# Performance work log

Hardware: AMD Instinct MI355X
Metric: run time of the kernel (lower is better)

The kernel has to match this reference:

```python
import jax, jax.numpy as jnp
import numpy as np

B, S, D, C_IN = 8, 1024, 512, 7
INNER = 2 * D              # mLSTM up-projection (proj_factor=2)
NH_M, DH_M = 4, INNER // 4 # mLSTM heads = n_heads//2
NH_S, DH_S = 8, D // 8     # sLSTM heads = n_heads
K_M, K_S = 7, 4            # conv kernels: enc_in, factor
FF = int(1.1 * D)          # sLSTM gated-FFN dim (proj_factor=1.1)
EPS = 1e-6
NEG = -1e30


def _ln(x, w):
    mu = x.mean(-1, keepdims=True)
    var = x.var(-1, keepdims=True)
    return (x - mu) * jax.lax.rsqrt(var + 1e-5) * w


def _headnorm(h, w):
    # h: [B,S,NH,DH] -> per-head groupnorm -> [B,S,NH*DH] * w
    mu = h.mean(-1, keepdims=True)
    var = h.var(-1, keepdims=True)
    hn = (h - mu) * jax.lax.rsqrt(var + 1e-5)
    b, s = h.shape[:2]
    return hn.reshape(b, s, -1) * w


def _causal_conv1d(x, w, b):
    # depthwise causal conv. x: [B,S,C], w: [C,k], b: [C]
    k = w.shape[1]
    xp = jnp.pad(x, ((0, 0), (k - 1, 0), (0, 0))).transpose(0, 2, 1)  # [B,C,S+k-1]
    y = jax.lax.conv_general_dilated(
        xp, w[:, None, :], (1,), 'VALID',
        dimension_numbers=('NCH', 'OIH', 'NCH'),
        feature_group_count=w.shape[0])
    return y.transpose(0, 2, 1) + b


def _mlstm_parallel(q, k, v, i_pre, f_pre):
    # q,k,v: [B,NH,S,DH]; i_pre,f_pre: [B,NH,S]. Stabilized parallel mLSTM cell.
    s = q.shape[2]
    logf = jax.nn.log_sigmoid(f_pre)
    cum = jnp.concatenate([jnp.zeros_like(logf[:, :, :1]), jnp.cumsum(logf, -1)], -1)  # [B,NH,S+1]
    dmat = cum[:, :, 1:, None] - cum[:, :, None, 1:]            # [B,NH,S,S]
    mask = jnp.tril(jnp.ones((s, s), bool))
    dmat = jnp.where(mask, dmat, NEG) + i_pre[:, :, None, :]    # add igate along keys
    m = dmat.max(-1, keepdims=True)                              # stabilizer
    Dm = jnp.exp(dmat - m)
    qk = jnp.einsum('bhqd,bhkd->bhqk', q, k) * (q.shape[-1] ** -0.5)
    C = qk * Dm
    n = jnp.maximum(jnp.abs(C.sum(-1, keepdims=True)), jnp.exp(-m)) + EPS
    return jnp.einsum('bhqk,bhkd->bhqd', C / n, v)               # [B,NH,S,DH]


def _forward(x_enc, x_mark_enc, x_dec, x_mark_dec, W_in, b_in,
             m_ln_w, m_Wup, m_bup, m_conv_w, m_conv_b, m_Wq, m_Wk, m_Wv,
             m_Wi, m_bi, m_Wf, m_bf, m_norm_w, m_skip, m_Wdown, m_bdown,
             s_ln_w, s_conv_w, s_conv_b, s_Wi, s_Wf, s_Wz, s_Wo,
             s_Ri, s_Rf, s_Rz, s_Ro, s_bi, s_bf, s_bz, s_bo, s_norm_w,
             s_ffn_ln_w, s_Wff_up, s_bff_up, s_Wff_down, s_bff_down,
             post_norm_w, W_out, b_out):
    b, s, _ = x_enc.shape
    x = x_enc @ W_in + b_in                                    # [B,S,D]

    # ---- block 0: mLSTM block ----
    res = x
    xn = _ln(x, m_ln_w)
    xm, z = jnp.split(xn @ m_Wup + m_bup, 2, axis=-1)          # each [B,S,INNER]
    conv = jax.nn.silu(_causal_conv1d(xm, m_conv_w, m_conv_b))
    qf, kf, vf = conv @ m_Wq, conv @ m_Wk, xm @ m_Wv
    gate_in = jnp.concatenate([qf, kf, vf], -1)                # [B,S,3*INNER]
    i_pre = (gate_in @ m_Wi + m_bi).transpose(0, 2, 1)         # [B,NH,S]
    f_pre = (gate_in @ m_Wf + m_bf).transpose(0, 2, 1)
    to_h = lambda t: t.reshape(b, s, NH_M, DH_M).transpose(0, 2, 1, 3)
    h = _mlstm_parallel(to_h(qf), to_h(kf), to_h(vf), i_pre, f_pre)
    h = h.transpose(0, 2, 1, 3)                                # [B,S,NH,DH]
    h = _headnorm(h, m_norm_w) + m_skip * conv                 # learnable skip
    x = res + (h * jax.nn.silu(z)) @ m_Wdown + m_bdown

    # ---- block 1: sLSTM block + gated FFN ----
    res = x
    xn = _ln(x, s_ln_w)
    conv = jax.nn.silu(_causal_conv1d(xn, s_conv_w, s_conv_b))
    gh = lambda t: t.reshape(b, s, NH_S, DH_S).transpose(1, 0, 2, 3)  # time-major
    gi, gf = gh(conv @ s_Wi + s_bi), gh(conv @ s_Wf + s_bf)
    gz, go = gh(xn @ s_Wz + s_bz), gh(xn @ s_Wo + s_bo)

    def step(carry, xs):
        c, n, m, hp = carry
        xi, xf, xz, xo = xs
        rec = lambda R: jnp.einsum('bhd,hde->bhe', hp, R)      # block-diag recurrent
        it, ft = xi + rec(s_Ri), xf + rec(s_Rf)
        zt, ot = xz + rec(s_Rz), xo + rec(s_Ro)
        m_new = jnp.maximum(ft + m, it)                        # exp-gate stabilizer
        ig = jnp.exp(it - m_new)
        fg = jnp.exp(ft + m - m_new)
        c_new = fg * c + ig * jnp.tanh(zt)
        n_new = fg * n + ig
        h_new = jax.nn.sigmoid(ot) * c_new / jnp.maximum(n_new, EPS)
        return (c_new, n_new, m_new, h_new), h_new

    z0 = jnp.zeros((b, NH_S, DH_S), x.dtype)
    _, hs = jax.lax.scan(step, (z0, z0, z0, z0), (gi, gf, gz, go))
    x = res + _headnorm(hs.transpose(1, 0, 2, 3), s_norm_w)

    res = x
    a, g = jnp.split(_ln(x, s_ffn_ln_w) @ s_Wff_up + s_bff_up, 2, axis=-1)
    x = res + (jax.nn.gelu(a) * g) @ s_Wff_down + s_bff_down

    x = _ln(x, post_norm_w)                                    # post-blocks norm
    return x @ W_out + b_out                                   # [B,S,7]


def setup_inputs() -> dict:
    key = jax.random.key(0)
    ks = iter(jax.random.split(key, 64))
    rn = lambda shape, sc=0.02: jax.random.normal(next(ks), shape, jnp.float32) * sc
    return {
        'x_enc': jax.random.normal(next(ks), (B, S, C_IN), jnp.float32),
        'x_mark_enc': jax.random.normal(next(ks), (B, S, 4), jnp.float32),
        'x_dec': jax.random.normal(next(ks), (B, S, C_IN), jnp.float32),
        'x_mark_dec': jax.random.normal(next(ks), (B, S, 4), jnp.float32),
        'W_in': rn((C_IN, D)), 'b_in': jnp.zeros((D,)),
        'm_ln_w': jnp.ones((D,)),
        'm_Wup': rn((D, 2 * INNER)), 'm_bup': jnp.zeros((2 * INNER,)),
        'm_conv_w': rn((INNER, K_M), 0.1), 'm_conv_b': jnp.zeros((INNER,)),
        'm_Wq': rn((INNER, INNER)), 'm_Wk': rn((INNER, INNER)), 'm_Wv': rn((INNER, INNER)),
        'm_Wi': rn((3 * INNER, NH_M)), 'm_bi': jnp.zeros((NH_M,)),
        'm_Wf': rn((3 * INNER, NH_M)), 'm_bf': jnp.full((NH_M,), 3.0),
        'm_norm_w': jnp.ones((INNER,)), 'm_skip': jnp.ones((INNER,)),
        'm_Wdown': rn((INNER, D)), 'm_bdown': jnp.zeros((D,)),
        's_ln_w': jnp.ones((D,)),
        's_conv_w': rn((D, K_S), 0.1), 's_conv_b': jnp.zeros((D,)),
        's_Wi': rn((D, D)), 's_Wf': rn((D, D)), 's_Wz': rn((D, D)), 's_Wo': rn((D, D)),
        's_Ri': rn((NH_S, DH_S, DH_S)), 's_Rf': rn((NH_S, DH_S, DH_S)),
        's_Rz': rn((NH_S, DH_S, DH_S)), 's_Ro': rn((NH_S, DH_S, DH_S)),
        's_bi': jnp.zeros((D,)), 's_bf': jnp.linspace(3.0, 6.0, D),
        's_bz': jnp.zeros((D,)), 's_bo': jnp.zeros((D,)),
        's_norm_w': jnp.ones((D,)),
        's_ffn_ln_w': jnp.ones((D,)),
        's_Wff_up': rn((D, 2 * FF)), 's_bff_up': jnp.zeros((2 * FF,)),
        's_Wff_down': rn((FF, D)), 's_bff_down': jnp.zeros((D,)),
        'post_norm_w': jnp.ones((D,)),
        'W_out': rn((D, C_IN)), 'b_out': jnp.zeros((C_IN,)),
    }


def reference(x_enc, x_mark_enc, x_dec, x_mark_dec, W_in, b_in,
              m_ln_w, m_Wup, m_bup, m_conv_w, m_conv_b, m_Wq, m_Wk, m_Wv,
              m_Wi, m_bi, m_Wf, m_bf, m_norm_w, m_skip, m_Wdown, m_bdown,
              s_ln_w, s_conv_w, s_conv_b, s_Wi, s_Wf, s_Wz, s_Wo,
              s_Ri, s_Rf, s_Rz, s_Ro, s_bi, s_bf, s_bz, s_bo, s_norm_w,
              s_ffn_ln_w, s_Wff_up, s_bff_up, s_Wff_down, s_bff_down,
              post_norm_w, W_out, b_out):
    return _forward(x_enc, x_mark_enc, x_dec, x_mark_dec, W_in, b_in,
                    m_ln_w, m_Wup, m_bup, m_conv_w, m_conv_b, m_Wq, m_Wk, m_Wv,
                    m_Wi, m_bi, m_Wf, m_bf, m_norm_w, m_skip, m_Wdown, m_bdown,
                    s_ln_w, s_conv_w, s_conv_b, s_Wi, s_Wf, s_Wz, s_Wo,
                    s_Ri, s_Rf, s_Rz, s_Ro, s_bi, s_bf, s_bz, s_bo, s_norm_w,
                    s_ffn_ln_w, s_Wff_up, s_bff_up, s_Wff_down, s_bff_down,
                    post_norm_w, W_out, b_out)
```

## Files before the change

### kernel.cpp

```cpp
#include <hip/hip_runtime.h>
#include <hip/hip_bf16.h>
#include <math.h>

typedef __hip_bfloat16 bf16;
typedef __attribute__((ext_vector_type(4))) float f32x4;
typedef __attribute__((ext_vector_type(8))) short bf16x8;
typedef __attribute__((ext_vector_type(8))) unsigned short u16x8;

#define DEV static __device__ __forceinline__

DEV float b2f(bf16 x) { return __bfloat162float(x); }
DEV bf16 f2b(float x) { return __float2bfloat16(x); }
DEV unsigned short f2us(float x) { bf16 h = __float2bfloat16(x); return *reinterpret_cast<unsigned short*>(&h); }
DEV float us2f(unsigned short u) { unsigned v = (unsigned)u << 16; float f; __builtin_memcpy(&f, &v, 4); return f; }

DEV float loadw(const void* p, size_t i, int bf) {
  return bf ? __bfloat162float(((const bf16*)p)[i]) : ((const float*)p)[i];
}

DEV float wredsum(float v) {
#pragma unroll
  for (int off = 32; off > 0; off >>= 1) v += __shfl_xor(v, off);
  return v;
}

DEV void gload_lds16(const void* g, void* l) {
  __builtin_amdgcn_global_load_lds((const __attribute__((address_space(1))) char*)g,
                                   (__attribute__((address_space(3))) char*)l, 16, 0, 0);
}

__global__ void k_flag(const unsigned* __restrict__ w1, int* flag) {
  if (threadIdx.x == 0 && blockIdx.x == 0) *flag = (*w1 == 0x3F800000u) ? 0 : 1;
}

__global__ void k_transpose(const void* __restrict__ W, int ldw, int colOff, bf16* __restrict__ Wt,
                            int K, int N, int Kpad, int Npad, const int* __restrict__ fp) {
  int bf = *fp;
  __shared__ float t[32][33];
  int n0 = blockIdx.x * 32, k0 = blockIdx.y * 32;
  int tx = threadIdx.x & 31, ty = threadIdx.x >> 5;
  for (int i = ty; i < 32; i += 8) {
    int k = k0 + i, n = n0 + tx;
    t[i][tx] = (k < K && n < N) ? loadw(W, (size_t)k * ldw + colOff + n, bf) : 0.f;
  }
  __syncthreads();
  for (int i = ty; i < 32; i += 8) {
    int n = n0 + i, k = k0 + tx;
    if (n < Npad && k < Kpad) Wt[(size_t)n * Kpad + k] = f2b(t[tx][i]);
  }
}

template <int RES>
__global__ __launch_bounds__(256) void k_gemm(
    const bf16* __restrict__ A, int lda, const bf16* __restrict__ Bt, int ldb,
    bf16* __restrict__ Cout, int ldc, const bf16* __restrict__ Res,
    const void* __restrict__ bias, int biasOff, int Nreal, int K,
    const int* __restrict__ fp) {
  int bf = *fp;
  __shared__ bf16 As[128 * 32];
  __shared__ bf16 Bs[128 * 32];
  int tid = threadIdx.x, wv = tid >> 6, lane = tid & 63;
  int mBase = blockIdx.y * 128, nBase = blockIdx.x * 128;
  int wm = (wv & 1) * 64, wn = (wv >> 1) * 64;
  f32x4 acc[4][4];
#pragma unroll
  for (int i = 0; i < 4; i++)
#pragma unroll
    for (int j = 0; j < 4; j++) acc[i][j] = 0.f;
  int r0 = (wv * 2) * 16 + (lane >> 2);
  int r1 = (wv * 2 + 1) * 16 + (lane >> 2);
  int cc = (lane & 3) * 8;
  const bf16* a0 = A + (size_t)(mBase + r0) * lda + cc;
  const bf16* a1 = A + (size_t)(mBase + r1) * lda + cc;
  const bf16* b0 = Bt + (size_t)(nBase + r0) * ldb + cc;
  const bf16* b1 = Bt + (size_t)(nBase + r1) * ldb + cc;
  for (int kt = 0; kt < K; kt += 32) {
    __syncthreads();
    gload_lds16(a0 + kt, As + (wv * 2) * 512);
    gload_lds16(a1 + kt, As + (wv * 2 + 1) * 512);
    gload_lds16(b0 + kt, Bs + (wv * 2) * 512);
    gload_lds16(b1 + kt, Bs + (wv * 2 + 1) * 512);
    __syncthreads();
    bf16x8 af[4], bfr[4];
#pragma unroll
    for (int i = 0; i < 4; i++) {
      af[i] = *(const bf16x8*)(As + (wm + i * 16 + (lane & 15)) * 32 + (lane >> 4) * 8);
      bfr[i] = *(const bf16x8*)(Bs + (wn + i * 16 + (lane & 15)) * 32 + (lane >> 4) * 8);
    }
#pragma unroll
    for (int i = 0; i < 4; i++)
#pragma unroll
      for (int j = 0; j < 4; j++)
        acc[i][j] = __builtin_amdgcn_mfma_f32_16x16x32_bf16(af[i], bfr[j], acc[i][j], 0, 0, 0);
  }
#pragma unroll
  for (int i = 0; i < 4; i++) {
#pragma unroll
    for (int j = 0; j < 4; j++) {
      int n = nBase + wn + j * 16 + (lane & 15);
      if (n < Nreal) {
        float bv = bias ? loadw(bias, biasOff + n, bf) : 0.f;
#pragma unroll
        for (int r = 0; r < 4; r++) {
          int m = mBase + wm + i * 16 + (lane >> 4) * 4 + r;
          float v = acc[i][j][r] + bv;
          if (RES) v += b2f(Res[(size_t)m * 512 + n]);
          Cout[(size_t)m * ldc + n] = f2b(v);
        }
      }
    }
  }
}

__global__ __launch_bounds__(256) void k_embed_ln(
    const void* __restrict__ xe, const void* __restrict__ Wi, const void* __restrict__ bi,
    const void* __restrict__ lw, bf16* __restrict__ x, bf16* __restrict__ xn,
    const int* __restrict__ fp) {
  int bf = *fp;
  int lane = threadIdx.x & 63, wv = threadIdx.x >> 6;
  size_t row = blockIdx.x * 4 + wv;
  float e[7];
#pragma unroll
  for (int c = 0; c < 7; c++) e[c] = loadw(xe, row * 7 + c, bf);
  float v[8];
#pragma unroll
  for (int j = 0; j < 8; j++) {
    int d = j * 64 + lane;
    float a = loadw(bi, d, bf);
#pragma unroll
    for (int c = 0; c < 7; c++) a += e[c] * loadw(Wi, c * 512 + d, bf);
    v[j] = a;
  }
  float s = 0, s2 = 0;
#pragma unroll
  for (int j = 0; j < 8; j++) { s += v[j]; s2 += v[j] * v[j]; }
  s = wredsum(s); s2 = wredsum(s2);
  float mu = s * (1.f / 512.f);
  float var = s2 * (1.f / 512.f) - mu * mu;
  float rq = rsqrtf(fmaxf(var, 0.f) + 1e-5f);
#pragma unroll
  for (int j = 0; j < 8; j++) {
    int d = j * 64 + lane;
    x[row * 512 + d] = f2b(v[j]);
    xn[row * 512 + d] = f2b((v[j] - mu) * rq * loadw(lw, d, bf));
  }
}

template <int KW>
__global__ void k_conv(const bf16* __restrict__ X, int ldx, int c4shift,
                       const void* __restrict__ cw, const void* __restrict__ cb,
                       bf16* __restrict__ out, int C, const int* __restrict__ fp) {
  int bf = *fp;
  int idx = blockIdx.x * 256 + threadIdx.x;
  int r = idx >> c4shift;
  int c4 = (idx & ((1 << c4shift) - 1)) * 4;
  int b = r >> 10, s = r & 1023;
  float a[4];
#pragma unroll
  for (int t = 0; t < 4; t++) a[t] = loadw(cb, c4 + t, bf);
#pragma unroll
  for (int j = 0; j < KW; j++) {
    int sj = s - (KW - 1) + j;
    if (sj >= 0) {
      const bf16* px = X + ((size_t)(b << 10) + sj) * ldx + c4;
#pragma unroll
      for (int t = 0; t < 4; t++) a[t] += b2f(px[t]) * loadw(cw, (c4 + t) * KW + j, bf);
    }
  }
#pragma unroll
  for (int t = 0; t < 4; t++) {
    float v = a[t];
    v = v / (1.f + __expf(-v));
    out[(size_t)r * C + c4 + t] = f2b(v);
  }
}

__global__ __launch_bounds__(256) void k_mgates(
    const bf16* __restrict__ qf, const bf16* __restrict__ kf, const bf16* __restrict__ vf,
    const void* __restrict__ Wi, const void* __restrict__ bi,
    const void* __restrict__ Wf, const void* __restrict__ bfv,
    float* __restrict__ ipre, float* __restrict__ fpre, const int* __restrict__ fp) {
  int bf = *fp;
  int lane = threadIdx.x & 63, wv = threadIdx.x >> 6;
  int row = blockIdx.x * 4 + wv;
  int b = row >> 10, s = row & 1023;
  float ai[4] = {0, 0, 0, 0}, af[4] = {0, 0, 0, 0};
  const bf16* srcs[3] = {qf + (size_t)row * 1024, kf + (size_t)row * 1024, vf + (size_t)row * 1024};
#pragma unroll
  for (int p = 0; p < 3; p++) {
    const bf16* sp = srcs[p];
#pragma unroll
    for (int it = 0; it < 16; it++) {
      int d = it * 64 + lane;
      float g = b2f(sp[d]);
      size_t wr = (size_t)(p * 1024 + d) * 4;
#pragma unroll
      for (int h = 0; h < 4; h++) {
        ai[h] += g * loadw(Wi, wr + h, bf);
        af[h] += g * loadw(Wf, wr + h, bf);
      }
    }
  }
#pragma unroll
  for (int h = 0; h < 4; h++) { ai[h] = wredsum(ai[h]); af[h] = wredsum(af[h]); }
  if (lane == 0) {
#pragma unroll
    for (int h = 0; h < 4; h++) {
      ipre[(size_t)(b * 4 + h) * 1024 + s] = ai[h] + loadw(bi, h, bf);
      fpre[(size_t)(b * 4 + h) * 1024 + s] = af[h] + loadw(bfv, h, bf);
    }
  }
}

__global__ void k_mprep(const float* __restrict__ ipre, const float* __restrict__ fpre,
                        float* __restrict__ aq, float* __restrict__ bk, float* __restrict__ bmax) {
  int bh = blockIdx.x, lane = threadIdx.x;
  float cum = 0.f, rmax = -3.4e38f;
  for (int t = 0; t < 1024; t += 64) {
    float f = fpre[(size_t)bh * 1024 + t + lane];
    float lf = fminf(f, 0.f) - log1pf(__expf(-fabsf(f)));
    float sc = lf;
#pragma unroll
    for (int off = 1; off < 64; off <<= 1) {
      float o = __shfl_up(sc, off);
      if (lane >= off) sc += o;
    }
    float a = cum + sc;
    float bkv = ipre[(size_t)bh * 1024 + t + lane] - a;
    float mx = bkv;
#pragma unroll
    for (int off = 1; off < 64; off <<= 1) {
      float o = __shfl_up(mx, off);
      if (lane >= off) mx = fmaxf(mx, o);
    }
    float m = fmaxf(rmax, mx);
    aq[(size_t)bh * 1024 + t + lane] = a;
    bk[(size_t)bh * 1024 + t + lane] = bkv;
    bmax[(size_t)bh * 1024 + t + lane] = m;
    cum += __shfl(sc, 63);
    rmax = fmaxf(rmax, __shfl(mx, 63));
  }
}

__global__ void k_vtrans(const bf16* __restrict__ vf, bf16* __restrict__ vt) {
  __shared__ bf16 t[32][33];
  int s0 = blockIdx.x * 32, d0 = blockIdx.y * 32, bh = blockIdx.z;
  int b = bh >> 2, h = bh & 3;
  int tx = threadIdx.x & 31, ty = threadIdx.x >> 5;
  for (int i = ty; i < 32; i += 8)
    t[i][tx] = vf[((size_t)(b << 10) + s0 + i) * 1024 + h * 256 + d0 + tx];
  __syncthreads();
  for (int i = ty; i < 32; i += 8)
    vt[((size_t)bh * 256 + d0 + i) * 1024 + s0 + tx] = t[tx][i];
}

__global__ __launch_bounds__(256) void k_mlstm(
    const bf16* __restrict__ qf, const bf16* __restrict__ kf, const bf16* __restrict__ vt,
    const float* __restrict__ aq, const float* __restrict__ bk, const float* __restrict__ bmax,
    const bf16* __restrict__ conv, const void* __restrict__ nw, const void* __restrict__ skip,
    bf16* __restrict__ y, const int* __restrict__ fp) {
  int bf = *fp;
  __shared__ bf16 Ks[64 * 256];
  __shared__ bf16 Vs[256 * 64];
  __shared__ unsigned short Ps[4][1024];
  int qt = blockIdx.x, bh = blockIdx.y;
  int b = bh >> 2, h = bh & 3;
  int tid = threadIdx.x, wv = tid >> 6, lane = tid & 63;
  size_t rowbase = (size_t)b << 10;
  int qw = qt * 64 + wv * 16;
  bf16x8 qreg[8];
  {
    const bf16* qp = qf + (rowbase + qw + (lane & 15)) * 1024 + h * 256 + (lane >> 4) * 8;
#pragma unroll
    for (int ck = 0; ck < 8; ck++) qreg[ck] = *(const bf16x8*)(qp + ck * 32);
  }
  float bmq[4], aqv[4];
#pragma unroll
  for (int r = 0; r < 4; r++) {
    int qg = qw + (lane >> 4) * 4 + r;
    bmq[r] = bmax[(size_t)bh * 1024 + qg];
    aqv[r] = aq[(size_t)bh * 1024 + qg];
  }
  f32x4 oacc[16];
#pragma unroll
  for (int i = 0; i < 16; i++) oacc[i] = 0.f;
  float rs[4] = {0, 0, 0, 0};
  int nkt = qt + 1;
  for (int kt = 0; kt < nkt; kt++) {
    int kbase = kt * 64;
    __syncthreads();
#pragma unroll
    for (int j = 0; j < 8; j++) {
      int ch = wv * 8 + j;
      int krow = ch * 2 + (lane >> 5);
      int sunit = (lane & 31) ^ (krow & 7);
      gload_lds16(kf + (rowbase + kbase + krow) * 1024 + h * 256 + sunit * 8, Ks + ch * 512);
    }
#pragma unroll
    for (int j = 0; j < 8; j++) {
      int ch = wv * 8 + j;
      int drow = ch * 8 + (lane >> 3);
      int sunit = (lane & 7) ^ (drow & 7);
      gload_lds16(vt + ((size_t)bh * 256 + drow) * 1024 + kbase + sunit * 8, Vs + ch * 512);
    }
    __syncthreads();
    float bkl = bk[(size_t)bh * 1024 + kbase + lane];
    f32x4 sacc[4];
#pragma unroll
    for (int kfg = 0; kfg < 4; kfg++) {
      int krow = kfg * 16 + (lane & 15);
      const char* kp = (const char*)Ks + krow * 512;
      int swz = (krow & 7) << 4;
      f32x4 sa = 0.f;
#pragma unroll
      for (int ck = 0; ck < 8; ck++) {
        int cb = (ck * 32 + (lane >> 4) * 8) * 2;
        bf16x8 bb = *(const bf16x8*)(kp + (cb ^ swz));
        sa = __builtin_amdgcn_mfma_f32_16x16x32_bf16(qreg[ck], bb, sa, 0, 0, 0);
      }
      sacc[kfg] = sa;
    }
    int qr0 = (lane >> 4) * 4;
#pragma unroll
    for (int kfg = 0; kfg < 4; kfg++) {
      int kloc = kfg * 16 + (lane & 15);
      float bkv = __shfl(bkl, kloc);
      int kglob = kbase + kloc;
#pragma unroll
      for (int r = 0; r < 4; r++) {
        int qloc = qr0 + r;
        int qglob = qt * 64 + wv * 16 + qloc;
        float p = sacc[kfg][r] * 0.0625f * __expf(bkv - bmq[r]);
        if (kglob > qglob) p = 0.f;
        rs[r] += p;
        int boff = qloc * 128 + ((kloc * 2) ^ ((qloc & 7) << 4));
        Ps[wv][boff >> 1] = f2us(p);
      }
    }
    __syncthreads();
#pragma unroll
    for (int kc = 0; kc < 2; kc++) {
      int qloc = lane & 15;
      int pboff = qloc * 128 + (((kc * 32 + (lane >> 4) * 8) * 2) ^ ((qloc & 7) << 4));
      bf16x8 pa = *(const bf16x8*)((const char*)Ps[wv] + pboff);
#pragma unroll
      for (int nf = 0; nf < 16; nf++) {
        int dr = nf * 16 + (lane & 15);
        int vboff = dr * 128 + (((kc * 32 + (lane >> 4) * 8) * 2) ^ ((dr & 7) << 4));
        bf16x8 vb = *(const bf16x8*)((const char*)Vs + vboff);
        oacc[nf] = __builtin_amdgcn_mfma_f32_16x16x32_bf16(pa, vb, oacc[nf], 0, 0, 0);
      }
    }
  }
#pragma unroll
  for (int r = 0; r < 4; r++) {
#pragma unroll
    for (int off = 1; off < 16; off <<= 1) rs[r] += __shfl_xor(rs[r], off);
  }
  float invn[4], mu[4], rqv[4];
#pragma unroll
  for (int r = 0; r < 4; r++) {
    float m = aqv[r] + bmq[r];
    float n = fmaxf(fabsf(rs[r]), __expf(-m)) + 1e-6f;
    invn[r] = 1.f / n;
  }
#pragma unroll
  for (int r = 0; r < 4; r++) {
    float s = 0.f, s2 = 0.f;
#pragma unroll
    for (int nf = 0; nf < 16; nf++) {
      float x = oacc[nf][r] * invn[r];
      s += x; s2 += x * x;
    }
#pragma unroll
    for (int off = 1; off < 16; off <<= 1) { s += __shfl_xor(s, off); s2 += __shfl_xor(s2, off); }
    mu[r] = s * (1.f / 256.f);
    float var = s2 * (1.f / 256.f) - mu[r] * mu[r];
    rqv[r] = rsqrtf(fmaxf(var, 0.f) + 1e-5f);
  }
#pragma unroll
  for (int nf = 0; nf < 16; nf++) {
    int dcol = h * 256 + nf * 16 + (lane & 15);
    float nwv = loadw(nw, dcol, bf);
    float skv = loadw(skip, dcol, bf);
#pragma unroll
    for (int r = 0; r < 4; r++) {
      size_t row = rowbase + qw + (lane >> 4) * 4 + r;
      float hn = (oacc[nf][r] * invn[r] - mu[r]) * rqv[r];
      float cv = b2f(conv[row * 1024 + dcol]);
      y[row * 1024 + dcol] = f2b(hn * nwv + skv * cv);
    }
  }
}

__global__ void k_zgate(bf16* __restrict__ y, const bf16* __restrict__ z) {
  size_t idx = ((size_t)blockIdx.x * 256 + threadIdx.x) * 8;
  u16x8 yv = *(const u16x8*)(y + idx);
  u16x8 zv = *(const u16x8*)(z + idx);
#pragma unroll
  for (int e = 0; e < 8; e++) {
    float f = us2f(yv[e]);
    float zz = us2f(zv[e]);
    f *= zz / (1.f + __expf(-zz));
    yv[e] = f2us(f);
  }
  *(u16x8*)(y + idx) = yv;
}

__global__ __launch_bounds__(256) void k_ln512(const bf16* __restrict__ X,
                                               const void* __restrict__ w,
                                               bf16* __restrict__ out,
                                               const int* __restrict__ fp) {
  int bf = *fp;
  int lane = threadIdx.x & 63, wv = threadIdx.x >> 6;
  size_t row = blockIdx.x * 4 + wv;
  float v[8];
  u16x8 q = *(const u16x8*)(X + row * 512 + lane * 8);
#pragma unroll
  for (int t = 0; t < 8; t++) v[t] = us2f(q[t]);
  float s = 0, s2 = 0;
#pragma unroll
  for (int t = 0; t < 8; t++) { s += v[t]; s2 += v[t] * v[t]; }
  s = wredsum(s); s2 = wredsum(s2);
  float mu = s * (1.f / 512.f), var = s2 * (1.f / 512.f) - mu * mu;
  float rq = rsqrtf(fmaxf(var, 0.f) + 1e-5f);
#pragma unroll
  for (int t = 0; t < 8; t++) {
    int d = lane * 8 + t;
    out[row * 512 + d] = f2b((v[t] - mu) * rq * loadw(w, d, bf));
  }
}

__global__ __launch_bounds__(256) void k_scan(
    const bf16* __restrict__ gif, const bf16* __restrict__ gzo,
    const void* __restrict__ Ri, const void* __restrict__ Rf,
    const void* __restrict__ Rz, const void* __restrict__ Ro,
    float* __restrict__ hs, const int* __restrict__ fp) {
  int bf = *fp;
  __shared__ __align__(16) float hprev[64];
  __shared__ float gout[4][64];
  int blk = blockIdx.x, b = blk >> 3, h = blk & 7;
  int wv = threadIdx.x >> 6, lane = threadIdx.x & 63;
  const void* Rsel = (wv == 0 ? Ri : wv == 1 ? Rf : wv == 2 ? Rz : Ro);
  float Rcol[64];
#pragma unroll
  for (int d = 0; d < 64; d++) Rcol[d] = loadw(Rsel, (size_t)h * 4096 + d * 64 + lane, bf);
  const bf16* gsel = (wv == 0) ? gif : (wv == 1) ? (gif + 512) : (wv == 2) ? gzo : (gzo + 512);
  size_t base = ((size_t)b << 10) * 1024 + h * 64 + lane;
  float c = 0.f, n = 0.f, m = 0.f;
  if (threadIdx.x < 64) hprev[threadIdx.x] = 0.f;
  __syncthreads();
  float xnext = b2f(gsel[base]);
  for (int s = 0; s < 1024; s++) {
    float xcur = xnext;
    if (s < 1023) xnext = b2f(gsel[base + (size_t)(s + 1) * 1024]);
    float a0 = 0, a1 = 0, a2 = 0, a3 = 0;
#pragma unroll
    for (int d = 0; d < 64; d += 4) {
      f32x4 hv = *(const f32x4*)(hprev + d);
      a0 += hv[0] * Rcol[d];
      a1 += hv[1] * Rcol[d + 1];
      a2 += hv[2] * Rcol[d + 2];
      a3 += hv[3] * Rcol[d + 3];
    }
    gout[wv][lane] = xcur + ((a0 + a1) + (a2 + a3));
    __syncthreads();
    float it = gout[0][lane], ft = gout[1][lane], zt = gout[2][lane], ot = gout[3][lane];
    float mn = fmaxf(ft + m, it);
    float ig = __expf(it - mn);
    float fg = __expf(ft + m - mn);
    float tz = 1.f - 2.f / (__expf(2.f * zt) + 1.f);
    c = fg * c + ig * tz;
    n = fg * n + ig;
    m = mn;
    float hv = (1.f / (1.f + __expf(-ot))) * c / fmaxf(n, 1e-6f);
    if (wv == 0) {
      hprev[lane] = hv;
      hs[(((size_t)b << 10) + s) * 512 + h * 64 + lane] = hv;
    }
    __syncthreads();
  }
}

__global__ __launch_bounds__(256) void k_snorm_ln(
    const bf16* __restrict__ x2, const float* __restrict__ hs, const void* __restrict__ nw,
    bf16* __restrict__ x3, const void* __restrict__ fw, bf16* __restrict__ xn3,
    const int* __restrict__ fp) {
  int bf = *fp;
  int lane = threadIdx.x & 63, wv = threadIdx.x >> 6;
  size_t row = blockIdx.x * 4 + wv;
  float v[8];
#pragma unroll
  for (int t = 0; t < 8; t += 4) {
    f32x4 q = *(const f32x4*)(hs + row * 512 + lane * 8 + t);
    v[t] = q[0]; v[t + 1] = q[1]; v[t + 2] = q[2]; v[t + 3] = q[3];
  }
  float s = 0, s2 = 0;
#pragma unroll
  for (int t = 0; t < 8; t++) { s += v[t]; s2 += v[t] * v[t]; }
#pragma unroll
  for (int off = 1; off < 8; off <<= 1) { s += __shfl_xor(s, off); s2 += __shfl_xor(s2, off); }
  float mu = s * (1.f / 64.f), var = s2 * (1.f / 64.f) - mu * mu;
  float rq = rsqrtf(fmaxf(var, 0.f) + 1e-5f);
  u16x8 qx = *(const u16x8*)(x2 + row * 512 + lane * 8);
  float xv[8];
  float ss = 0, ss2 = 0;
#pragma unroll
  for (int t = 0; t < 8; t++) {
    int d = lane * 8 + t;
    float val = us2f(qx[t]) + (v[t] - mu) * rq * loadw(nw, d, bf);
    xv[t] = val;
    x3[row * 512 + d] = f2b(val);
    ss += val; ss2 += val * val;
  }
  ss = wredsum(ss); ss2 = wredsum(ss2);
  float mu2 = ss * (1.f / 512.f), var2 = ss2 * (1.f / 512.f) - mu2 * mu2;
  float rq2 = rsqrtf(fmaxf(var2, 0.f) + 1e-5f);
#pragma unroll
  for (int t = 0; t < 8; t++) {
    int d = lane * 8 + t;
    xn3[row * 512 + d] = f2b((xv[t] - mu2) * rq2 * loadw(fw, d, bf));
  }
}

__global__ void k_gelugate(const bf16* __restrict__ a, const bf16* __restrict__ g,
                           bf16* __restrict__ y2) {
  int idx = blockIdx.x * 256 + threadIdx.x;
  int r = idx / 576, j = idx - r * 576;
  float v = 0.f;
  if (j < 563) {
    float av = b2f(a[(size_t)r * 576 + j]);
    float gv = b2f(g[(size_t)r * 576 + j]);
    float u = 0.7978845608028654f * (av + 0.044715f * av * av * av);
    float th = 1.f - 2.f / (__expf(2.f * u) + 1.f);
    v = 0.5f * av * (1.f + th) * gv;
  }
  y2[(size_t)r * 576 + j] = f2b(v);
}

__global__ __launch_bounds__(256) void k_final(
    const bf16* __restrict__ x4, const void* __restrict__ pw,
    const void* __restrict__ Wo, const void* __restrict__ bo, void* __restrict__ out,
    const int* __restrict__ fp) {
  int bf = *fp;
  int lane = threadIdx.x & 63, wv = threadIdx.x >> 6;
  size_t row = blockIdx.x * 4 + wv;
  float v[8];
  u16x8 q = *(const u16x8*)(x4 + row * 512 + lane * 8);
#pragma unroll
  for (int t = 0; t < 8; t++) v[t] = us2f(q[t]);
  float s = 0, s2 = 0;
#pragma unroll
  for (int t = 0; t < 8; t++) { s += v[t]; s2 += v[t] * v[t]; }
  s = wredsum(s); s2 = wredsum(s2);
  float mu = s * (1.f / 512.f), var = s2 * (1.f / 512.f) - mu * mu;
  float rq = rsqrtf(fmaxf(var, 0.f) + 1e-5f);
  float o[7] = {0, 0, 0, 0, 0, 0, 0};
#pragma unroll
  for (int t = 0; t < 8; t++) {
    int d = lane * 8 + t;
    float xn = (v[t] - mu) * rq * loadw(pw, d, bf);
#pragma unroll
    for (int cc = 0; cc < 7; cc++) o[cc] += xn * loadw(Wo, d * 7 + cc, bf);
  }
#pragma unroll
  for (int cc = 0; cc < 7; cc++) o[cc] = wredsum(o[cc]);
  if (lane == 0) {
#pragma unroll
    for (int cc = 0; cc < 7; cc++) {
      float r = o[cc] + loadw(bo, cc, bf);
      if (bf) ((bf16*)out)[row * 7 + cc] = f2b(r);
      else ((float*)out)[row * 7 + cc] = r;
    }
  }
}

extern "C" void kernel_launch(void* const* d_in, const int* in_sizes, int n_in,
                              void* d_out, int out_size, void* d_ws, size_t ws_size,
                              hipStream_t stream) {
  const void* x_enc = d_in[0];
  const void* W_in = d_in[4];
  const void* b_in = d_in[5];
  const void* m_ln_w = d_in[6];
  const void* m_Wup = d_in[7];
  const void* m_bup = d_in[8];
  const void* m_conv_w = d_in[9];
  const void* m_conv_b = d_in[10];
  const void* m_Wq = d_in[11];
  const void* m_Wk = d_in[12];
  const void* m_Wv = d_in[13];
  const void* m_Wi = d_in[14];
  const void* m_bi = d_in[15];
  const void* m_Wf = d_in[16];
  const void* m_bf = d_in[17];
  const void* m_norm_w = d_in[18];
  const void* m_skip = d_in[19];
  const void* m_Wdown = d_in[20];
  const void* m_bdown = d_in[21];
  const void* s_ln_w = d_in[22];
  const void* s_conv_w = d_in[23];
  const void* s_conv_b = d_in[24];
  const void* s_Wi = d_in[25];
  const void* s_Wf = d_in[26];
  const void* s_Wz = d_in[27];
  const void* s_Wo = d_in[28];
  const void* s_Ri = d_in[29];
  const void* s_Rf = d_in[30];
  const void* s_Rz = d_in[31];
  const void* s_Ro = d_in[32];
  const void* s_bi = d_in[33];
  const void* s_bf = d_in[34];
  const void* s_bz = d_in[35];
  const void* s_bo = d_in[36];
  const void* s_norm_w = d_in[37];
  const void* s_ffn_ln_w = d_in[38];
  const void* s_Wff_up = d_in[39];
  const void* s_bff_up = d_in[40];
  const void* s_Wff_down = d_in[41];
  const void* s_bff_down = d_in[42];
  const void* post_norm_w = d_in[43];
  const void* W_out = d_in[44];
  const void* b_out = d_in[45];

  char* ws = (char*)d_ws;
  size_t off = 0;
  auto alloc = [&](size_t bytes) { void* p = ws + off; off += (bytes + 255) & ~(size_t)255; return p; };
  const size_t M = 8192;

  int* flag = (int*)alloc(256);
  float* ipre = (float*)alloc(32 * 1024 * 4);
  float* fpre = (float*)alloc(32 * 1024 * 4);
  float* aqB = (float*)alloc(32 * 1024 * 4);
  float* bkB = (float*)alloc(32 * 1024 * 4);
  float* bmB = (float*)alloc(32 * 1024 * 4);
  bf16* R1 = (bf16*)alloc(M * 512 * 2);
  bf16* R2 = (bf16*)alloc(M * 512 * 2);
  bf16* T1 = (bf16*)alloc(M * 512 * 2);
  bf16* SA = (bf16*)alloc(M * 1024 * 2);
  bf16* SB = (bf16*)alloc(M * 1024 * 2);
  bf16* SC = (bf16*)alloc(M * 1024 * 2);
  bf16* SD = (bf16*)alloc(M * 1024 * 2);
  bf16* SE = (bf16*)alloc(M * 1024 * 2);
  bf16* ARENA = (bf16*)alloc((size_t)8 * 1024 * 1024);
  (void)ws_size;

  bf16* wt_up = ARENA;
  bf16* wt_q = ARENA + (size_t)2048 * 512;
  bf16* wt_k = wt_q + (size_t)1024 * 1024;
  bf16* wt_v = wt_k + (size_t)1024 * 1024;
  bf16* wt_down = ARENA;
  bf16* wt_i = ARENA + (size_t)512 * 1024;
  bf16* wt_f = wt_i + (size_t)512 * 512;
  bf16* wt_z = wt_f + (size_t)512 * 512;
  bf16* wt_o = wt_z + (size_t)512 * 512;
  bf16* wt_ffa = ARENA;
  bf16* wt_ffg = wt_ffa + (size_t)640 * 512;
  bf16* wt_ffdn = wt_ffg + (size_t)640 * 512;

  k_flag<<<1, 64, 0, stream>>>((const unsigned*)m_ln_w, flag);

  k_transpose<<<dim3(64, 16), 256, 0, stream>>>(m_Wup, 2048, 0, wt_up, 512, 2048, 512, 2048, flag);
  k_transpose<<<dim3(32, 32), 256, 0, stream>>>(m_Wq, 1024, 0, wt_q, 1024, 1024, 1024, 1024, flag);
  k_transpose<<<dim3(32, 32), 256, 0, stream>>>(m_Wk, 1024, 0, wt_k, 1024, 1024, 1024, 1024, flag);
  k_transpose<<<dim3(32, 32), 256, 0, stream>>>(m_Wv, 1024, 0, wt_v, 1024, 1024, 1024, 1024, flag);

  k_embed_ln<<<2048, 256, 0, stream>>>(x_enc, W_in, b_in, m_ln_w, R1, T1, flag);
  k_gemm<0><<<dim3(8, 64), 256, 0, stream>>>(T1, 512, wt_up, 512, SA, 1024, nullptr, m_bup, 0, 1024, 512, flag);
  k_conv<7><<<8192, 256, 0, stream>>>(SA, 1024, 8, m_conv_w, m_conv_b, SB, 1024, flag);
  k_gemm<0><<<dim3(8, 64), 256, 0, stream>>>(SB, 1024, wt_q, 1024, SC, 1024, nullptr, nullptr, 0, 1024, 1024, flag);
  k_gemm<0><<<dim3(8, 64), 256, 0, stream>>>(SB, 1024, wt_k, 1024, SD, 1024, nullptr, nullptr, 0, 1024, 1024, flag);
  k_gemm<0><<<dim3(8, 64), 256, 0, stream>>>(SA, 1024, wt_v, 1024, SE, 1024, nullptr, nullptr, 0, 1024, 1024, flag);
  k_mgates<<<2048, 256, 0, stream>>>(SC, SD, SE, m_Wi, m_bi, m_Wf, m_bf, ipre, fpre, flag);
  k_mprep<<<32, 64, 0, stream>>>(ipre, fpre, aqB, bkB, bmB);
  bf16* vt = SA;
  k_vtrans<<<dim3(32, 8, 32), 256, 0, stream>>>(SE, vt);
  k_mlstm<<<dim3(16, 32), 256, 0, stream>>>(SC, SD, vt, aqB, bkB, bmB, SB, m_norm_w, m_skip, SB, flag);
  k_gemm<0><<<dim3(8, 64), 256, 0, stream>>>(T1, 512, wt_up + (size_t)1024 * 512, 512, SE, 1024, nullptr, m_bup, 1024, 1024, 512, flag);
  k_zgate<<<4096, 256, 0, stream>>>(SB, SE);
  k_transpose<<<dim3(16, 32), 256, 0, stream>>>(m_Wdown, 512, 0, wt_down, 1024, 512, 1024, 512, flag);
  k_transpose<<<dim3(16, 16), 256, 0, stream>>>(s_Wi, 512, 0, wt_i, 512, 512, 512, 512, flag);
  k_transpose<<<dim3(16, 16), 256, 0, stream>>>(s_Wf, 512, 0, wt_f, 512, 512, 512, 512, flag);
  k_transpose<<<dim3(16, 16), 256, 0, stream>>>(s_Wz, 512, 0, wt_z, 512, 512, 512, 512, flag);
  k_transpose<<<dim3(16, 16), 256, 0, stream>>>(s_Wo, 512, 0, wt_o, 512, 512, 512, 512, flag);
  k_gemm<1><<<dim3(4, 64), 256, 0, stream>>>(SB, 1024, wt_down, 1024, R2, 512, R1, m_bdown, 0, 512, 1024, flag);

  k_ln512<<<2048, 256, 0, stream>>>(R2, s_ln_w, T1, flag);
  k_conv<4><<<4096, 256, 0, stream>>>(T1, 512, 7, s_conv_w, s_conv_b, SE, 512, flag);
  k_gemm<0><<<dim3(4, 64), 256, 0, stream>>>(SE, 512, wt_i, 512, SA, 1024, nullptr, s_bi, 0, 512, 512, flag);
  k_gemm<0><<<dim3(4, 64), 256, 0, stream>>>(SE, 512, wt_f, 512, SA + 512, 1024, nullptr, s_bf, 0, 512, 512, flag);
  k_gemm<0><<<dim3(4, 64), 256, 0, stream>>>(T1, 512, wt_z, 512, SC, 1024, nullptr, s_bz, 0, 512, 512, flag);
  k_gemm<0><<<dim3(4, 64), 256, 0, stream>>>(T1, 512, wt_o, 512, SC + 512, 1024, nullptr, s_bo, 0, 512, 512, flag);
  float* hsF = (float*)SD;
  k_scan<<<64, 256, 0, stream>>>(SA, SC, s_Ri, s_Rf, s_Rz, s_Ro, hsF, flag);
  k_snorm_ln<<<2048, 256, 0, stream>>>(R2, hsF, s_norm_w, R1, s_ffn_ln_w, T1, flag);

  k_transpose<<<dim3(20, 16), 256, 0, stream>>>(s_Wff_up, 1126, 0, wt_ffa, 512, 563, 512, 640, flag);
  k_transpose<<<dim3(20, 16), 256, 0, stream>>>(s_Wff_up, 1126, 563, wt_ffg, 512, 563, 512, 640, flag);
  k_transpose<<<dim3(16, 18), 256, 0, stream>>>(s_Wff_down, 512, 0, wt_ffdn, 563, 512, 576, 512, flag);
  k_gemm<0><<<dim3(5, 64), 256, 0, stream>>>(T1, 512, wt_ffa, 512, SE, 576, nullptr, s_bff_up, 0, 563, 512, flag);
  k_gemm<0><<<dim3(5, 64), 256, 0, stream>>>(T1, 512, wt_ffg, 512, SA, 576, nullptr, s_bff_up, 563, 563, 512, flag);
  k_gelugate<<<18432, 256, 0, stream>>>(SE, SA, SB);
  k_gemm<1><<<dim3(4, 64), 256, 0, stream>>>(SB, 576, wt_ffdn, 576, R2, 512, R1, s_bff_down, 0, 512, 576, flag);

  k_final<<<2048, 256, 0, stream>>>(R2, post_norm_w, W_out, b_out, d_out, flag);
}
```

Measured before the change: 1.729 ms.

## Restructure sLSTM scan to split recurrent dot product across lanes with shuffles

The per-step recurrent matvec is repartitioned so that each thread computes all four gates for one output unit over a 16-element slice of the hidden state. Partial sums are then combined with cross-lane shuffles, which replaces the gate exchange through shared memory. A double-buffered hidden-state array removes one of the two block barriers per timestep, and the hs store moves to a different lane group. This is meant to shorten the serial latency of each step, at the cost of extra shuffle instructions and four gate inputs loaded per thread.

```diff
diff --git a/kernel.cpp b/kernel.cpp
--- a/kernel.cpp
+++ b/kernel.cpp
@@ -437,35 +437,59 @@
     const void* __restrict__ Rz, const void* __restrict__ Ro,
     float* __restrict__ hs, const int* __restrict__ fp) {
   int bf = *fp;
-  __shared__ __align__(16) float hprev[64];
-  __shared__ float gout[4][64];
+  __shared__ __align__(16) float hbuf[2][64];
   int blk = blockIdx.x, b = blk >> 3, h = blk & 7;
-  int wv = threadIdx.x >> 6, lane = threadIdx.x & 63;
-  const void* Rsel = (wv == 0 ? Ri : wv == 1 ? Rf : wv == 2 ? Rz : Ro);
-  float Rcol[64];
-#pragma unroll
-  for (int d = 0; d < 64; d++) Rcol[d] = loadw(Rsel, (size_t)h * 4096 + d * 64 + lane, bf);
-  const bf16* gsel = (wv == 0) ? gif : (wv == 1) ? (gif + 512) : (wv == 2) ? gzo : (gzo + 512);
-  size_t base = ((size_t)b << 10) * 1024 + h * 64 + lane;
+  int w = threadIdx.x >> 6, lane = threadIdx.x & 63;
+  int e_loc = lane & 15, d_blk = lane >> 4;
+  int e = w * 16 + e_loc;
+  int d0 = d_blk * 16;
+  float Rg[4][16];
+  const void* Rp[4] = {Ri, Rf, Rz, Ro};
+#pragma unroll
+  for (int g = 0; g < 4; g++)
+#pragma unroll
+    for (int d = 0; d < 16; d++)
+      Rg[g][d] = loadw(Rp[g], (size_t)h * 4096 + (size_t)(d0 + d) * 64 + e, bf);
+  size_t base = ((size_t)b << 10) * 1024 + h * 64 + e;
+  size_t hsbase = (((size_t)b << 10)) * 512 + h * 64 + e;
   float c = 0.f, n = 0.f, m = 0.f;
-  if (threadIdx.x < 64) hprev[threadIdx.x] = 0.f;
+  if (threadIdx.x < 64) { hbuf[0][threadIdx.x] = 0.f; hbuf[1][threadIdx.x] = 0.f; }
   __syncthreads();
-  float xnext = b2f(gsel[base]);
+  float xi = b2f(gif[base]), xf = b2f(gif[base + 512]);
+  float xz = b2f(gzo[base]), xo = b2f(gzo[base + 512]);
+  int p = 0;
   for (int s = 0; s < 1024; s++) {
-    float xcur = xnext;
-    if (s < 1023) xnext = b2f(gsel[base + (size_t)(s + 1) * 1024]);
-    float a0 = 0, a1 = 0, a2 = 0, a3 = 0;
-#pragma unroll
-    for (int d = 0; d < 64; d += 4) {
-      f32x4 hv = *(const f32x4*)(hprev + d);
-      a0 += hv[0] * Rcol[d];
-      a1 += hv[1] * Rcol[d + 1];
-      a2 += hv[2] * Rcol[d + 2];
-      a3 += hv[3] * Rcol[d + 3];
-    }
-    gout[wv][lane] = xcur + ((a0 + a1) + (a2 + a3));
-    __syncthreads();
-    float it = gout[0][lane], ft = gout[1][lane], zt = gout[2][lane], ot = gout[3][lane];
+    float hv[16];
+#pragma unroll
+    for (int t = 0; t < 16; t += 4) {
+      f32x4 q = *(const f32x4*)(&hbuf[p][d0 + t]);
+      hv[t] = q[0]; hv[t + 1] = q[1]; hv[t + 2] = q[2]; hv[t + 3] = q[3];
+    }
+    float ci = xi, cf = xf, cz = xz, co = xo;
+    float a[4] = {0.f, 0.f, 0.f, 0.f};
+    if (s < 1023) {
+      size_t nb = base + (size_t)(s + 1) * 1024;
+      xi = b2f(gif[nb]); xf = b2f(gif[nb + 512]);
+      xz = b2f(gzo[nb]); xo = b2f(gzo[nb + 512]);
+    }
+#pragma unroll
+    for (int g = 0; g < 4; g++) {
+      float p0 = 0, p1 = 0, p2 = 0, p3 = 0;
+#pragma unroll
+      for (int d = 0; d < 16; d += 4) {
+        p0 += hv[d] * Rg[g][d];
+        p1 += hv[d + 1] * Rg[g][d + 1];
+        p2 += hv[d + 2] * Rg[g][d + 2];
+        p3 += hv[d + 3] * Rg[g][d + 3];
+      }
+      a[g] += (p0 + p1) + (p2 + p3);
+    }
+#pragma unroll
+    for (int g = 0; g < 4; g++) {
+      a[g] += __shfl_xor(a[g], 16);
+      a[g] += __shfl_xor(a[g], 32);
+    }
+    float it = a[0] + ci, ft = a[1] + cf, zt = a[2] + cz, ot = a[3] + co;
     float mn = fmaxf(ft + m, it);
     float ig = __expf(it - mn);
     float fg = __expf(ft + m - mn);
@@ -473,11 +497,10 @@
     c = fg * c + ig * tz;
     n = fg * n + ig;
     m = mn;
-    float hv = (1.f / (1.f + __expf(-ot))) * c / fmaxf(n, 1e-6f);
-    if (wv == 0) {
-      hprev[lane] = hv;
-      hs[(((size_t)b << 10) + s) * 512 + h * 64 + lane] = hv;
-    }
+    float hvn = (1.f / (1.f + __expf(-ot))) * c / fmaxf(n, 1e-6f);
+    if (d_blk == 0) hbuf[p ^ 1][e] = hvn;
+    if (d_blk == 1) hs[hsbase + (size_t)s * 512] = hvn;
+    p ^= 1;
     __syncthreads();
   }
 }
```

Measured after the change: 1.669 ms. 3.5% less time.
